# Kernel tuning notes

Hardware: AMD Instinct MI355X
Metric: run time of the kernel (lower is better)

Reference implementation:

```python
import jax, jax.numpy as jnp
import numpy as np

N_NODES = 100000
N_EDGES = 1200000
IN_FEATS = 128
HIDDEN = 64
OUT_FEATS = 40


def setup_inputs() -> dict:
    key = jax.random.key(0)
    k1, k2, k3, k4, k5 = jax.random.split(key, 5)
    x = jax.random.normal(k1, (N_NODES, IN_FEATS), dtype=jnp.float32)
    edge_index = jax.random.randint(k2, (2, N_EDGES), 0, N_NODES, dtype=jnp.int64)
    W1 = jax.random.normal(k3, (IN_FEATS, HIDDEN), dtype=jnp.float32) * (1.0 / np.sqrt(IN_FEATS))
    b1 = jnp.zeros((HIDDEN,), dtype=jnp.float32)
    W2 = jax.random.normal(k4, (HIDDEN, HIDDEN), dtype=jnp.float32) * (1.0 / np.sqrt(HIDDEN))
    b2 = jnp.zeros((HIDDEN,), dtype=jnp.float32)
    Wc = jax.random.normal(k5, (HIDDEN, OUT_FEATS), dtype=jnp.float32) * (1.0 / np.sqrt(HIDDEN))
    bc = jnp.zeros((OUT_FEATS,), dtype=jnp.float32)
    return {"x": x, "edge_index": edge_index, "W1": W1, "b1": b1,
            "W2": W2, "b2": b2, "Wc": Wc, "bc": bc}


def _gcn_norm(edge_index, n_nodes):
    # add self-loops, then symmetric normalization deg^{-1/2}[src] * deg^{-1/2}[dst]
    loops = jnp.arange(n_nodes, dtype=edge_index.dtype)
    src = jnp.concatenate([edge_index[0], loops])
    dst = jnp.concatenate([edge_index[1], loops])
    ones = jnp.ones(src.shape[0], dtype=jnp.float32)
    deg = jax.ops.segment_sum(ones, dst, num_segments=n_nodes)  # in-degree incl. self-loop
    dinv = jnp.where(deg > 0, jax.lax.rsqrt(deg), 0.0)
    norm = dinv[src] * dinv[dst]  # [E+N]
    return src, dst, norm


def _gcn_conv(h, W, b, src, dst, norm, n_nodes):
    h = h @ W                          # [N, F_out] dense transform first (PyG GCNConv)
    msg = h[src] * norm[:, None]       # gather + normalize, [E+N, F_out]
    out = jax.ops.segment_sum(msg, dst, num_segments=n_nodes)  # scatter-add
    return out + b


def reference(x, edge_index, W1, b1, W2, b2, Wc, bc):
    n = x.shape[0]
    src, dst, norm = _gcn_norm(edge_index, n)
    # dropout is identity in eval mode
    h = jax.nn.relu(_gcn_conv(x, W1, b1, src, dst, norm, n))
    embedding = _gcn_conv(h, W2, b2, src, dst, norm, n)
    logits = embedding @ Wc + bc
    soft_label = jax.nn.softmax(logits, axis=1)
    hard_label = jnp.argmax(soft_label, axis=1)
    return (logits, embedding, soft_label, hard_label)
```

## Files before the change

### kernel.cpp

```cpp
#include <hip/hip_runtime.h>
#include <hip/hip_bf16.h>
#include <math.h>

typedef __hip_bfloat16 bf16;
typedef __attribute__((ext_vector_type(8))) short bf16x8;
typedef __attribute__((ext_vector_type(4))) float f32x4;

__device__ __forceinline__ float loadf(const void* p, size_t i, bool f32m) {
    return f32m ? ((const float*)p)[i]
                : __bfloat162float(((const bf16*)p)[i]);
}
__device__ __forceinline__ void storef(void* p, size_t i, float v, bool f32m) {
    if (f32m) ((float*)p)[i] = v;
    else      ((bf16*)p)[i] = __float2bfloat16(v);
}
__device__ __forceinline__ int ldidx(const int* w, size_t e, bool e64, size_t E, int row) {
    return e64 ? w[2 * (row * E + e)] : w[row * E + e];
}

__device__ __forceinline__ unsigned short f2bf(float f) {
    unsigned u = __float_as_uint(f);
    unsigned r = (u + 0x7FFFu + ((u >> 16) & 1u)) >> 16;
    return (unsigned short)r;
}
__device__ __forceinline__ float bf2f(unsigned short h) {
    return __uint_as_float(((unsigned)h) << 16);
}

__global__ void k_detect(const void* x, const int* ei, float* flags) {
    int lane = threadIdx.x;
    const unsigned short* hx = (const unsigned short*)x;
    unsigned short u = hx[2 * lane];
    int ex = (u >> 7) & 0xFF;
    bool tame = (ex >= 117 && ex <= 136);
    unsigned long long mt = __ballot(tame);
    unsigned long long mz = __ballot(ei[2 * lane + 1] != 0);
    if (lane == 0) {
        flags[0] = (__popcll(mt) >= 48) ? 0.0f : 1.0f;
        flags[1] = (mz == 0ULL) ? 1.0f : 0.0f;
    }
}


__global__ void k_zero_small(int* __restrict__ p, int m) {
    int i = blockIdx.x * 256 + threadIdx.x;
    if (i < m) p[i] = 0;
}

#define SCB_EPT 16

__global__ __launch_bounds__(256) void k_bucket_hist(const int* __restrict__ ei,
                                                     const float* __restrict__ flags,
                                                     int* __restrict__ bcnt, int E, int NB) {
    __shared__ int lcnt[512];
    bool e64 = flags[1] > 0.5f;
    int tid = threadIdx.x;
    for (int i = tid; i < NB; i += 256) lcnt[i] = 0;
    __syncthreads();
    int base = blockIdx.x * 256 * SCB_EPT;
#pragma unroll
    for (int j = 0; j < SCB_EPT; ++j) {
        int e = base + j * 256 + tid;
        if (e < E) atomicAdd(&lcnt[ldidx(ei, e, e64, E, 1) >> 8], 1);
    }
    __syncthreads();
    for (int i = tid; i < NB; i += 256) {
        int c = lcnt[i];
        if (c) atomicAdd(&bcnt[i], c);
    }
}

__global__ __launch_bounds__(512) void k_scan_buckets(const int* __restrict__ bcnt,
                                                      int* __restrict__ bbase,
                                                      int* __restrict__ bcur, int NB) {
    __shared__ int sh[512];
    int tid = threadIdx.x;
    int v = (tid < NB) ? bcnt[tid] : 0;
    sh[tid] = v;
    __syncthreads();
    for (int off = 1; off < 512; off <<= 1) {
        int t = (tid >= off) ? sh[tid - off] : 0;
        __syncthreads();
        sh[tid] += t;
        __syncthreads();
    }
    if (tid < NB) {
        int ex = sh[tid] - v;
        bbase[tid] = ex;
        bcur[tid] = ex;
    }
    if (tid == 0) bbase[NB] = sh[511];
}

__global__ __launch_bounds__(256) void k_bucket_scatter(const int* __restrict__ ei,
                                                        const float* __restrict__ flags,
                                                        int* __restrict__ bcur,
                                                        int2* __restrict__ recs,
                                                        int E, int NB) {
    __shared__ int lcnt[512], lrank[512], lbase[512];
    bool e64 = flags[1] > 0.5f;
    int tid = threadIdx.x;
    for (int i = tid; i < NB; i += 256) { lcnt[i] = 0; lrank[i] = 0; }
    __syncthreads();
    int base = blockIdx.x * 256 * SCB_EPT;
    int s[SCB_EPT], d[SCB_EPT];
#pragma unroll
    for (int j = 0; j < SCB_EPT; ++j) {
        int e = base + j * 256 + tid;
        if (e < E) {
            s[j] = ldidx(ei, e, e64, E, 0);
            d[j] = ldidx(ei, e, e64, E, 1);
            atomicAdd(&lcnt[d[j] >> 8], 1);
        } else d[j] = -1;
    }
    __syncthreads();
    for (int i = tid; i < NB; i += 256) {
        int c = lcnt[i];
        lbase[i] = c ? atomicAdd(&bcur[i], c) : 0;
    }
    __syncthreads();
#pragma unroll
    for (int j = 0; j < SCB_EPT; ++j) {
        if (d[j] >= 0) {
            int b = d[j] >> 8;
            int r = atomicAdd(&lrank[b], 1);
            recs[lbase[b] + r] = make_int2(s[j], d[j]);
        }
    }
}

__global__ __launch_bounds__(256) void k_bucket_csr(const int2* __restrict__ recs,
                                                    const int* __restrict__ bbase,
                                                    int* __restrict__ rowptr,
                                                    float* __restrict__ dinv,
                                                    int* __restrict__ srcs,
                                                    int n, int E) {
    __shared__ int lcnt[256];
    __shared__ int lcur[256];
    int b = blockIdx.x, tid = threadIdx.x;
    int e0 = bbase[b], e1 = bbase[b + 1];
    lcnt[tid] = 0;
    __syncthreads();
    for (int i = e0 + tid; i < e1; i += 256)
        atomicAdd(&lcnt[recs[i].y & 255], 1);
    __syncthreads();
    int c = lcnt[tid];
    lcur[tid] = c;
    __syncthreads();
    for (int off = 1; off < 256; off <<= 1) {
        int t = (tid >= off) ? lcur[tid - off] : 0;
        __syncthreads();
        lcur[tid] += t;
        __syncthreads();
    }
    int rp = bbase[b] + lcur[tid] - c;
    int node = (b << 8) + tid;
    if (node < n) {
        rowptr[node] = rp;
        dinv[node] = rsqrtf((float)(c + 1));
    }
    lcur[tid] = rp;
    __syncthreads();
    for (int i = e0 + tid; i < e1; i += 256) {
        int2 r = recs[i];
        int pos = atomicAdd(&lcur[r.y & 255], 1);
        srcs[pos] = r.x;
    }
    if (b == 0 && tid == 0) rowptr[n] = E;
}

template <int K, bool XALWAYSF32>
__global__ __launch_bounds__(256) void k_gconv_mfma(const void* __restrict__ Xa,
                                                    const void* __restrict__ Xb,
                                                    const void* __restrict__ W,
                                                    const float* __restrict__ flags,
                                                    const float* __restrict__ rowscale,
                                                    float* __restrict__ out, int n) {
    constexpr int KP = K + 8;
    __shared__ __align__(16) unsigned short wh[64 * KP];
    __shared__ __align__(16) unsigned short wlo[64 * KP];
    bool f32m = flags[0] > 0.5f;
    const void* X = f32m ? Xa : Xb;
    bool xf32 = XALWAYSF32 || f32m;
    int tid = threadIdx.x;

    if (f32m) {
        for (int i = tid * 4; i < K * 64; i += 1024) {
            int k = i >> 6, c = i & 63;
            float4 v = *(const float4*)((const float*)W + i);
            float vv[4] = {v.x, v.y, v.z, v.w};
#pragma unroll
            for (int q = 0; q < 4; ++q) {
                unsigned short h = f2bf(vv[q]);
                unsigned short l = f2bf(vv[q] - bf2f(h));
                wh [(c + q) * KP + k] = h;
                wlo[(c + q) * KP + k] = l;
            }
        }
    } else {
        for (int i = tid; i < K * 64; i += 256) {
            int k = i >> 6, c = i & 63;
            wh [c * KP + k] = ((const unsigned short*)W)[i];
            wlo[c * KP + k] = 0;
        }
    }
    __syncthreads();

    int lane = tid & 63, wv = tid >> 6;
    int r0 = blockIdx.x * 64 + wv * 16;
    int mrow = lane & 15, kgrp = lane >> 4;
    int row = r0 + mrow;
    bool rok = (row < n);

    f32x4 acc[4];
#pragma unroll
    for (int ct = 0; ct < 4; ++ct) acc[ct] = (f32x4){0.0f, 0.0f, 0.0f, 0.0f};

    const float*          xrf = (const float*)X          + (size_t)(rok ? row : 0) * K;
    const unsigned short* xrb = (const unsigned short*)X + (size_t)(rok ? row : 0) * K;

#pragma unroll
    for (int ks = 0; ks < K / 32; ++ks) {
        int kb = ks * 32 + kgrp * 8;
        bf16x8 ahi = {0, 0, 0, 0, 0, 0, 0, 0};
        bf16x8 alo = {0, 0, 0, 0, 0, 0, 0, 0};
        if (rok) {
            if (xf32) {
                float4 v0 = *(const float4*)(xrf + kb);
                float4 v1 = *(const float4*)(xrf + kb + 4);
                float fv[8] = {v0.x, v0.y, v0.z, v0.w, v1.x, v1.y, v1.z, v1.w};
#pragma unroll
                for (int j = 0; j < 8; ++j) {
                    unsigned short h = f2bf(fv[j]);
                    ahi[j] = (short)h;
                    alo[j] = (short)f2bf(fv[j] - bf2f(h));
                }
            } else {
                ahi = *(const bf16x8*)(xrb + kb);
            }
        }
#pragma unroll
        for (int ct = 0; ct < 4; ++ct) {
            int c = ct * 16 + mrow;
            bf16x8 bhi = *(const bf16x8*)&wh [c * KP + kb];
            bf16x8 blo = *(const bf16x8*)&wlo[c * KP + kb];
            acc[ct] = __builtin_amdgcn_mfma_f32_16x16x32_bf16(ahi, bhi, acc[ct], 0, 0, 0);
            acc[ct] = __builtin_amdgcn_mfma_f32_16x16x32_bf16(ahi, blo, acc[ct], 0, 0, 0);
            acc[ct] = __builtin_amdgcn_mfma_f32_16x16x32_bf16(alo, bhi, acc[ct], 0, 0, 0);
        }
    }

    float sc[4];
    int obase = r0 + kgrp * 4;
#pragma unroll
    for (int r = 0; r < 4; ++r)
        sc[r] = (obase + r < n) ? rowscale[obase + r] : 0.0f;
#pragma unroll
    for (int ct = 0; ct < 4; ++ct) {
#pragma unroll
        for (int r = 0; r < 4; ++r) {
            int orow = obase + r;
            if (orow < n)
                out[(size_t)orow * 64 + ct * 16 + mrow] = acc[ct][r] * sc[r];
        }
    }
}

template <int EP>
__global__ __launch_bounds__(256) void k_agg(const float* __restrict__ t,
                                             const float* __restrict__ dinv,
                                             const int* __restrict__ rowptr,
                                             const int* __restrict__ srcs,
                                             const void* __restrict__ bias,
                                             const float* __restrict__ flags,
                                             void* __restrict__ d_out, size_t emb_base,
                                             float* __restrict__ B_ws, int n) {
    bool f32m = flags[0] > 0.5f;
    int wvid = (blockIdx.x * 256 + threadIdx.x) >> 6;
    int lane = threadIdx.x & 63;
    int grp = lane >> 4;
    int col4 = lane & 15;
    int v0 = wvid * 2;
    int v1 = v0 + 1;
    if (v0 >= n) return;
    bool has1 = (v1 < n);

    float4 bias4;
    if (f32m) {
        bias4 = ((const float4*)bias)[col4];
    } else {
        const bf16* bp = (const bf16*)bias + col4 * 4;
        bias4.x = __bfloat162float(bp[0]); bias4.y = __bfloat162float(bp[1]);
        bias4.z = __bfloat162float(bp[2]); bias4.w = __bfloat162float(bp[3]);
    }

    float dvA = dinv[v0];
    float dvB = has1 ? dinv[v1] : 0.0f;
    int e0a = rowptr[v0], e1a = rowptr[v0 + 1];
    int e0b = has1 ? rowptr[v1] : 0;
    int e1b = has1 ? rowptr[v1 + 1] : 0;
    int degA = e1a - e0a + 1;
    int degB = has1 ? (e1b - e0b + 1) : 0;
    int degMax = degA > degB ? degA : degB;

    float4 accA = {0, 0, 0, 0}, accB = {0, 0, 0, 0};

    for (int base = 0; base < degMax; base += 64) {
        int jA = base + lane;
        int sA_l = -1;
        if (jA == 0) sA_l = v0;
        else if (jA < degA) sA_l = srcs[e0a + jA - 1];
        int sB_l = -1;
        if (has1) {
            int jB = base + lane;
            if (jB == 0) sB_l = v1;
            else if (jB < degB) sB_l = srcs[e0b + jB - 1];
        }
        int rem = degMax - base;
        int mq = rem < 64 ? rem : 64;

        for (int q = 0; q < mq; q += 16) {
            int sa[4], sb[4];
#pragma unroll
            for (int u = 0; u < 4; ++u) {
                int idx = q + 4 * u + grp;
                sa[u] = __shfl(sA_l, idx, 64);
                sb[u] = __shfl(sB_l, idx, 64);
            }
            float4 va[4], vb[4];
#pragma unroll
            for (int u = 0; u < 4; ++u) {
                va[u] = make_float4(0, 0, 0, 0);
                if (sa[u] >= 0)
                    va[u] = *((const float4*)(t + ((size_t)sa[u] << 6)) + col4);
                vb[u] = make_float4(0, 0, 0, 0);
                if (sb[u] >= 0)
                    vb[u] = *((const float4*)(t + ((size_t)sb[u] << 6)) + col4);
            }
#pragma unroll
            for (int u = 0; u < 4; ++u) {
                accA.x += va[u].x; accA.y += va[u].y; accA.z += va[u].z; accA.w += va[u].w;
                accB.x += vb[u].x; accB.y += vb[u].y; accB.z += vb[u].z; accB.w += vb[u].w;
            }
        }
    }

#pragma unroll
    for (int off = 16; off < 64; off <<= 1) {
        accA.x += __shfl_xor(accA.x, off, 64);
        accA.y += __shfl_xor(accA.y, off, 64);
        accA.z += __shfl_xor(accA.z, off, 64);
        accA.w += __shfl_xor(accA.w, off, 64);
        accB.x += __shfl_xor(accB.x, off, 64);
        accB.y += __shfl_xor(accB.y, off, 64);
        accB.z += __shfl_xor(accB.z, off, 64);
        accB.w += __shfl_xor(accB.w, off, 64);
    }

    int v = -1; float4 acc; float dv = 0.0f;
    if (grp == 0) { v = v0; acc = accA; dv = dvA; }
    else if (grp == 1 && has1) { v = v1; acc = accB; dv = dvB; }
    if (v >= 0) {
        acc.x = acc.x * dv + bias4.x;
        acc.y = acc.y * dv + bias4.y;
        acc.z = acc.z * dv + bias4.z;
        acc.w = acc.w * dv + bias4.w;
        if (EP == 0) {
            acc.x = fmaxf(acc.x, 0.0f); acc.y = fmaxf(acc.y, 0.0f);
            acc.z = fmaxf(acc.z, 0.0f); acc.w = fmaxf(acc.w, 0.0f);
        }
        size_t ob = (size_t)v * 64 + col4 * 4;
        if (f32m) {
            *(float4*)((float*)d_out + emb_base + ob) = acc;
        } else {
            *(float4*)&B_ws[ob] = acc;
            if (EP == 1) {
                __hip_bfloat162 h0, h1;
                h0.x = __float2bfloat16(acc.x); h0.y = __float2bfloat16(acc.y);
                h1.x = __float2bfloat16(acc.z); h1.y = __float2bfloat16(acc.w);
                __hip_bfloat162* p = (__hip_bfloat162*)((bf16*)d_out + emb_base + ob);
                p[0] = h0; p[1] = h1;
            }
        }
    }
}


__device__ __forceinline__ void store_row40(void* out, size_t base, const float* a, bool f32m) {
    if (f32m) {
        float4* p = (float4*)((float*)out + base);
#pragma unroll
        for (int q = 0; q < 10; ++q) {
            float4 st = {a[q * 4 + 0], a[q * 4 + 1], a[q * 4 + 2], a[q * 4 + 3]};
            p[q] = st;
        }
    } else {
        __hip_bfloat162* p = (__hip_bfloat162*)((bf16*)out + base);
#pragma unroll
        for (int i = 0; i < 20; ++i) {
            __hip_bfloat162 h;
            h.x = __float2bfloat16(a[2 * i]);
            h.y = __float2bfloat16(a[2 * i + 1]);
            p[i] = h;
        }
    }
}

__global__ __launch_bounds__(256) void k_classifier(const float* __restrict__ flags,
                                                    const void* __restrict__ Wc,
                                                    const void* __restrict__ bc,
                                                    void* __restrict__ out,
                                                    size_t emb_base, size_t soft_base,
                                                    size_t hard_base,
                                                    const float* __restrict__ B_ws,
                                                    int n) {
    __shared__ __align__(16) float wcs[64 * 40];
    __shared__ __align__(16) float bcs[40];
    bool f32m = flags[0] > 0.5f;
    const float* emb = f32m ? ((const float*)out + emb_base) : B_ws;
    int tid = threadIdx.x;

    if (f32m) {
        for (int i = tid * 4; i < 64 * 40; i += 1024)
            *(float4*)&wcs[i] = *(const float4*)((const float*)Wc + i);
    } else {
        for (int i = tid; i < 64 * 40; i += 256)
            wcs[i] = __bfloat162float(((const bf16*)Wc)[i]);
    }
    if (tid < 40) bcs[tid] = loadf(bc, tid, f32m);
    __syncthreads();

    int node = blockIdx.x * 256 + tid;
    if (node >= n) return;

    float acc[40];
#pragma unroll
    for (int q = 0; q < 10; ++q) {
        float4 b4 = *(const float4*)&bcs[q * 4];
        acc[q * 4 + 0] = b4.x; acc[q * 4 + 1] = b4.y;
        acc[q * 4 + 2] = b4.z; acc[q * 4 + 3] = b4.w;
    }

    const float4* erow = (const float4*)(emb + (size_t)node * 64);
#pragma unroll 2
    for (int j = 0; j < 16; ++j) {
        float4 e4 = erow[j];
        float ev[4] = {e4.x, e4.y, e4.z, e4.w};
#pragma unroll
        for (int kk = 0; kk < 4; ++kk) {
            float e = ev[kk];
            const float4* wr = (const float4*)&wcs[(j * 4 + kk) * 40];
#pragma unroll
            for (int q = 0; q < 10; ++q) {
                float4 w = wr[q];
                acc[q * 4 + 0] = fmaf(e, w.x, acc[q * 4 + 0]);
                acc[q * 4 + 1] = fmaf(e, w.y, acc[q * 4 + 1]);
                acc[q * 4 + 2] = fmaf(e, w.z, acc[q * 4 + 2]);
                acc[q * 4 + 3] = fmaf(e, w.w, acc[q * 4 + 3]);
            }
        }
    }

    store_row40(out, (size_t)node * 40, acc, f32m);

    float m0 = acc[0], m1 = acc[1], m2 = acc[2], m3 = acc[3];
#pragma unroll
    for (int q = 1; q < 10; ++q) {
        m0 = fmaxf(m0, acc[q * 4 + 0]); m1 = fmaxf(m1, acc[q * 4 + 1]);
        m2 = fmaxf(m2, acc[q * 4 + 2]); m3 = fmaxf(m3, acc[q * 4 + 3]);
    }
    float m = fmaxf(fmaxf(m0, m1), fmaxf(m2, m3));

    int bi = 63;
#pragma unroll
    for (int c = 0; c < 40; ++c)
        if (acc[c] == m && c < bi) bi = c;

    float s = 0.0f;
#pragma unroll
    for (int c = 0; c < 40; ++c) {
        float e = expf(acc[c] - m);
        acc[c] = e;
        s += e;
    }
    float rs = 1.0f / s;
#pragma unroll
    for (int c = 0; c < 40; ++c) acc[c] *= rs;

    store_row40(out, soft_base + (size_t)node * 40, acc, f32m);
    storef(out, hard_base + node, (float)bi, f32m);
}

extern "C" void kernel_launch(void* const* d_in, const int* in_sizes, int n_in,
                              void* d_out, int out_size, void* d_ws, size_t ws_size,
                              hipStream_t stream) {
    const void* x  = d_in[0];
    const int*  ei = (const int*)d_in[1];
    const void* W1 = d_in[2];
    const void* b1 = d_in[3];
    const void* W2 = d_in[4];
    const void* b2 = d_in[5];
    const void* Wc = d_in[6];
    const void* bc = d_in[7];

    const int n = in_sizes[0] / 128;
    const int E = in_sizes[1] / 2;
    const int NB = (n + 255) / 256;

    float* ws    = (float*)d_ws;
    const size_t npad = (((size_t)n + 1023) / 1024) * 1024;
    const size_t Epad = (((size_t)E + 255) / 256) * 256;
    float* flags  = ws;
    int*   bcnt   = (int*)(ws + 256);
    int*   bbase  = (int*)(ws + 768);
    int*   bcur   = (int*)(ws + 1536);
    int*   rowptr = (int*)(ws + 2048);
    float* dinv   = (float*)(rowptr + npad);
    int*   srcs   = (int*)(dinv + npad);
    float* A      = (float*)(srcs + Epad);
    float* B_ws   = A + (size_t)n * 64;
    int2*  recs   = (int2*)B_ws;

    const size_t emb_base  = (size_t)n * 40;
    const size_t soft_base = (size_t)n * 104;
    const size_t hard_base = (size_t)n * 144;
    float* h1_f32m = (float*)d_out + emb_base;

    const int gS  = (E + 256 * SCB_EPT - 1) / (256 * SCB_EPT);
    const int gG  = (n + 63) / 64;
    const int gW  = (n + 7) / 8;
    const int gC  = (n + 255) / 256;

    k_detect<<<1, 64, 0, stream>>>(x, ei, flags);

    k_zero_small<<<2, 256, 0, stream>>>(bcnt, 512);
    k_bucket_hist<<<gS, 256, 0, stream>>>(ei, flags, bcnt, E, NB);
    k_scan_buckets<<<1, 512, 0, stream>>>(bcnt, bbase, bcur, NB);
    k_bucket_scatter<<<gS, 256, 0, stream>>>(ei, flags, bcur, recs, E, NB);
    k_bucket_csr<<<NB, 256, 0, stream>>>(recs, bbase, rowptr, dinv, srcs, n, E);

    k_gconv_mfma<128, false><<<gG, 256, 0, stream>>>(x, x, W1, flags, dinv, A, n);
    k_agg<0><<<gW, 256, 0, stream>>>(A, dinv, rowptr, srcs, b1, flags,
                                     d_out, emb_base, B_ws, n);

    k_gconv_mfma<64, true><<<gG, 256, 0, stream>>>(h1_f32m, B_ws, W2, flags, dinv, A, n);
    k_agg<1><<<gW, 256, 0, stream>>>(A, dinv, rowptr, srcs, b2, flags,
                                     d_out, emb_base, B_ws, n);

    k_classifier<<<gC, 256, 0, stream>>>(flags, Wc, bc, d_out,
                                         emb_base, soft_base, hard_base, B_ws, n);
}
```

Measured before the change: 313.1 us.

## Assign one node per 16-lane group in GCN aggregation kernel

The aggregation kernel now gives each 16-lane quarter-wave its own destination node, so a wave covers four nodes instead of two. Each group reads its node's neighbor indices, broadcasts them with shuffles inside the group, and accumulates neighbor rows directly starting from the self-loop row. This removes the cross-group shuffle reduction and the wasted edge slots that came from padding to the larger degree of a node pair. In exchange, each wave now waits for the largest degree among its four nodes, and fewer loads are in flight per iteration. The launch grid is halved to match.

```diff
diff --git a/kernel.cpp b/kernel.cpp
--- a/kernel.cpp
+++ b/kernel.cpp
@@ -279,108 +279,67 @@
     int wvid = (blockIdx.x * 256 + threadIdx.x) >> 6;
     int lane = threadIdx.x & 63;
     int grp = lane >> 4;
-    int col4 = lane & 15;
-    int v0 = wvid * 2;
-    int v1 = v0 + 1;
-    if (v0 >= n) return;
-    bool has1 = (v1 < n);
+    int sub = lane & 15;
+    int v = wvid * 4 + grp;
+    if (v >= n) return;
+
+    float dv = dinv[v];
+    int e0 = rowptr[v], e1 = rowptr[v + 1];
+    int deg = e1 - e0;
+
+    float4 acc = *(const float4*)(t + ((size_t)v << 6) + sub * 4);
+
+    for (int base = 0; base < deg; base += 16) {
+        int idx = base + sub;
+        int sid = (idx < deg) ? srcs[e0 + idx] : -1;
+        int cnt = deg - base; if (cnt > 16) cnt = 16;
+        for (int j = 0; j < cnt; j += 4) {
+            int gb = grp * 16 + j;
+            int s0 = __shfl(sid, gb + 0, 64);
+            int s1 = __shfl(sid, gb + 1, 64);
+            int s2 = __shfl(sid, gb + 2, 64);
+            int s3 = __shfl(sid, gb + 3, 64);
+            float4 r0 = {0, 0, 0, 0}, r1 = {0, 0, 0, 0}, r2 = {0, 0, 0, 0}, r3 = {0, 0, 0, 0};
+            if (s0 >= 0) r0 = *(const float4*)(t + ((size_t)s0 << 6) + sub * 4);
+            if (s1 >= 0) r1 = *(const float4*)(t + ((size_t)s1 << 6) + sub * 4);
+            if (s2 >= 0) r2 = *(const float4*)(t + ((size_t)s2 << 6) + sub * 4);
+            if (s3 >= 0) r3 = *(const float4*)(t + ((size_t)s3 << 6) + sub * 4);
+            acc.x += (r0.x + r1.x) + (r2.x + r3.x);
+            acc.y += (r0.y + r1.y) + (r2.y + r3.y);
+            acc.z += (r0.z + r1.z) + (r2.z + r3.z);
+            acc.w += (r0.w + r1.w) + (r2.w + r3.w);
+        }
+    }
 
     float4 bias4;
     if (f32m) {
-        bias4 = ((const float4*)bias)[col4];
+        bias4 = ((const float4*)bias)[sub];
     } else {
-        const bf16* bp = (const bf16*)bias + col4 * 4;
+        const bf16* bp = (const bf16*)bias + sub * 4;
         bias4.x = __bfloat162float(bp[0]); bias4.y = __bfloat162float(bp[1]);
         bias4.z = __bfloat162float(bp[2]); bias4.w = __bfloat162float(bp[3]);
     }
 
-    float dvA = dinv[v0];
-    float dvB = has1 ? dinv[v1] : 0.0f;
-    int e0a = rowptr[v0], e1a = rowptr[v0 + 1];
-    int e0b = has1 ? rowptr[v1] : 0;
-    int e1b = has1 ? rowptr[v1 + 1] : 0;
-    int degA = e1a - e0a + 1;
-    int degB = has1 ? (e1b - e0b + 1) : 0;
-    int degMax = degA > degB ? degA : degB;
-
-    float4 accA = {0, 0, 0, 0}, accB = {0, 0, 0, 0};
-
-    for (int base = 0; base < degMax; base += 64) {
-        int jA = base + lane;
-        int sA_l = -1;
-        if (jA == 0) sA_l = v0;
-        else if (jA < degA) sA_l = srcs[e0a + jA - 1];
-        int sB_l = -1;
-        if (has1) {
-            int jB = base + lane;
-            if (jB == 0) sB_l = v1;
-            else if (jB < degB) sB_l = srcs[e0b + jB - 1];
-        }
-        int rem = degMax - base;
-        int mq = rem < 64 ? rem : 64;
-
-        for (int q = 0; q < mq; q += 16) {
-            int sa[4], sb[4];
-#pragma unroll
-            for (int u = 0; u < 4; ++u) {
-                int idx = q + 4 * u + grp;
-                sa[u] = __shfl(sA_l, idx, 64);
-                sb[u] = __shfl(sB_l, idx, 64);
-            }
-            float4 va[4], vb[4];
-#pragma unroll
-            for (int u = 0; u < 4; ++u) {
-                va[u] = make_float4(0, 0, 0, 0);
-                if (sa[u] >= 0)
-                    va[u] = *((const float4*)(t + ((size_t)sa[u] << 6)) + col4);
-                vb[u] = make_float4(0, 0, 0, 0);
-                if (sb[u] >= 0)
-                    vb[u] = *((const float4*)(t + ((size_t)sb[u] << 6)) + col4);
-            }
-#pragma unroll
-            for (int u = 0; u < 4; ++u) {
-                accA.x += va[u].x; accA.y += va[u].y; accA.z += va[u].z; accA.w += va[u].w;
-                accB.x += vb[u].x; accB.y += vb[u].y; accB.z += vb[u].z; accB.w += vb[u].w;
-            }
-        }
-    }
-
-#pragma unroll
-    for (int off = 16; off < 64; off <<= 1) {
-        accA.x += __shfl_xor(accA.x, off, 64);
-        accA.y += __shfl_xor(accA.y, off, 64);
-        accA.z += __shfl_xor(accA.z, off, 64);
-        accA.w += __shfl_xor(accA.w, off, 64);
-        accB.x += __shfl_xor(accB.x, off, 64);
-        accB.y += __shfl_xor(accB.y, off, 64);
-        accB.z += __shfl_xor(accB.z, off, 64);
-        accB.w += __shfl_xor(accB.w, off, 64);
-    }
-
-    int v = -1; float4 acc; float dv = 0.0f;
-    if (grp == 0) { v = v0; acc = accA; dv = dvA; }
-    else if (grp == 1 && has1) { v = v1; acc = accB; dv = dvB; }
-    if (v >= 0) {
-        acc.x = acc.x * dv + bias4.x;
-        acc.y = acc.y * dv + bias4.y;
-        acc.z = acc.z * dv + bias4.z;
-        acc.w = acc.w * dv + bias4.w;
-        if (EP == 0) {
-            acc.x = fmaxf(acc.x, 0.0f); acc.y = fmaxf(acc.y, 0.0f);
-            acc.z = fmaxf(acc.z, 0.0f); acc.w = fmaxf(acc.w, 0.0f);
-        }
-        size_t ob = (size_t)v * 64 + col4 * 4;
-        if (f32m) {
-            *(float4*)((float*)d_out + emb_base + ob) = acc;
-        } else {
-            *(float4*)&B_ws[ob] = acc;
-            if (EP == 1) {
-                __hip_bfloat162 h0, h1;
-                h0.x = __float2bfloat16(acc.x); h0.y = __float2bfloat16(acc.y);
-                h1.x = __float2bfloat16(acc.z); h1.y = __float2bfloat16(acc.w);
-                __hip_bfloat162* p = (__hip_bfloat162*)((bf16*)d_out + emb_base + ob);
-                p[0] = h0; p[1] = h1;
-            }
+    float4 o;
+    o.x = acc.x * dv + bias4.x;
+    o.y = acc.y * dv + bias4.y;
+    o.z = acc.z * dv + bias4.z;
+    o.w = acc.w * dv + bias4.w;
+    if (EP == 0) {
+        o.x = fmaxf(o.x, 0.0f); o.y = fmaxf(o.y, 0.0f);
+        o.z = fmaxf(o.z, 0.0f); o.w = fmaxf(o.w, 0.0f);
+    }
+    size_t ob = ((size_t)v << 6) + sub * 4;
+    if (f32m) {
+        *(float4*)((float*)d_out + emb_base + ob) = o;
+    } else {
+        *(float4*)&B_ws[ob] = o;
+        if (EP == 1) {
+            __hip_bfloat162 h0, h1;
+            h0.x = __float2bfloat16(o.x); h0.y = __float2bfloat16(o.y);
+            h1.x = __float2bfloat16(o.z); h1.y = __float2bfloat16(o.w);
+            __hip_bfloat162* p = (__hip_bfloat162*)((bf16*)d_out + emb_base + ob);
+            p[0] = h0; p[1] = h1;
         }
     }
 }
@@ -528,7 +487,7 @@
 
     const int gS  = (E + 256 * SCB_EPT - 1) / (256 * SCB_EPT);
     const int gG  = (n + 63) / 64;
-    const int gW  = (n + 7) / 8;
+    const int gW  = (n + 15) / 16;
     const int gC  = (n + 255) / 256;
 
     k_detect<<<1, 64, 0, stream>>>(x, ei, flags);
```

Result: no change. 314.6 us (+0.5%).
